# Kernel tuning notes

Measured on AMD Instinct MI355X. Metric: run time of the kernel, lower is better.

## Reference

```python
import jax, jax.numpy as jnp
import numpy as np

UNITS = 512
IN_DIM = 256
BATCH = 256
SEQ = 256


def setup_inputs() -> dict:
    key = jax.random.key(0)
    ks = jax.random.split(key, 9)
    s = lambda fan_in: 1.0 / np.sqrt(fan_in)
    inputs = jax.random.normal(ks[0], (BATCH, SEQ, IN_DIM), dtype=jnp.float32)
    # layer 0: input dim IN_DIM -> UNITS; layer 1: UNITS -> UNITS
    W0 = jax.random.normal(ks[1], (IN_DIM, 4 * UNITS), dtype=jnp.float32) * s(IN_DIM)
    U0 = jax.random.normal(ks[2], (UNITS, 4 * UNITS), dtype=jnp.float32) * s(UNITS)
    b0 = jnp.zeros((4 * UNITS,), dtype=jnp.float32)
    W1 = jax.random.normal(ks[3], (UNITS, 4 * UNITS), dtype=jnp.float32) * s(UNITS)
    U1 = jax.random.normal(ks[4], (UNITS, 4 * UNITS), dtype=jnp.float32) * s(UNITS)
    b1 = jnp.zeros((4 * UNITS,), dtype=jnp.float32)
    Wfc = jax.random.normal(ks[5], (UNITS, 1), dtype=jnp.float32) * s(UNITS)
    bfc = jnp.zeros((1,), dtype=jnp.float32)
    return {"inputs": inputs, "W0": W0, "U0": U0, "b0": b0,
            "W1": W1, "U1": U1, "b1": b1, "Wfc": Wfc, "bfc": bfc}


def _lstm_cell(x, h, c, W, U, b):
    # Keras LSTMCell gate order: i, f, g(candidate), o
    z = x @ W + h @ U + b  # [B, 4u]
    i, f, g, o = jnp.split(z, 4, axis=-1)
    c_new = jax.nn.sigmoid(f) * c + jax.nn.sigmoid(i) * jnp.tanh(g)
    h_new = jax.nn.sigmoid(o) * jnp.tanh(c_new)
    return h_new, c_new


def reference(inputs, W0, U0, b0, W1, U1, b1, Wfc, bfc):
    B = inputs.shape[0]
    u = U0.shape[0]
    zeros = jnp.zeros((B, u), dtype=inputs.dtype)
    init = (zeros, zeros, zeros, zeros)  # h0, c0, h1, c1

    def step(carry, x_t):
        h0, c0, h1, c1 = carry
        h0, c0 = _lstm_cell(x_t, h0, c0, W0, U0, b0)
        h1, c1 = _lstm_cell(h0, h1, c1, W1, U1, b1)
        return (h0, c0, h1, c1), None

    xs = jnp.swapaxes(inputs, 0, 1)  # [T, B, D]
    (h0, c0, h1, c1), _ = jax.lax.scan(step, init, xs)
    # RNN returns last output of top cell; Dense(1) head
    return h1 @ Wfc + bfc  # [B, 1]
```

## Files before the change

kernel.cpp:

```cpp
#include <hip/hip_runtime.h>
#include <hip/hip_bf16.h>

#define BATCH 256
#define SEQT  256
#define INDIM 256
#define UNITS 512
#define GCOLS 2048
#define BLOCKT 256

typedef __attribute__((ext_vector_type(8))) __bf16 bf16x8;
typedef __attribute__((ext_vector_type(4))) float  f32x4;

#define AS1 __attribute__((address_space(1)))
#define AS3 __attribute__((address_space(3)))

__device__ __forceinline__ void load_lds16_coh(const void* gsrc, void* ldst) {
    __builtin_amdgcn_global_load_lds((AS1 void*)gsrc, (AS3 void*)ldst, 16, 0, 0x11);
}

__device__ __forceinline__ float sigf(float x) { return 1.0f / (1.0f + __expf(-x)); }

__device__ __forceinline__ float tanhfast(float x) {
    float e = __expf(-2.0f * fabsf(x));
    float t = (1.0f - e) / (1.0f + e);
    return x < 0.0f ? -t : t;
}

__device__ __forceinline__ unsigned short f2bf(float f) {
    unsigned u = __float_as_uint(f);
    u += 0x7fffu + ((u >> 16) & 1u);
    return (unsigned short)(u >> 16);
}

__device__ __forceinline__ void st_coh(unsigned long long* p, unsigned long long v) {
    __hip_atomic_store(p, v, __ATOMIC_RELAXED, __HIP_MEMORY_SCOPE_AGENT);
}

__device__ __forceinline__ void group_barrier(unsigned* cnt, unsigned target) {
    asm volatile("s_waitcnt vmcnt(0)" ::: "memory");
    __syncthreads();
    if (threadIdx.x == 0) {
        __hip_atomic_fetch_add(cnt, 1u, __ATOMIC_RELAXED, __HIP_MEMORY_SCOPE_AGENT);
        while (__hip_atomic_load(cnt, __ATOMIC_RELAXED, __HIP_MEMORY_SCOPE_AGENT) < target)
            __builtin_amdgcn_s_sleep(1);
    }
    __syncthreads();
}

template <int LAYER>
__device__ void run_lstm(const float* __restrict__ X,
                         const float* __restrict__ Wx, const float* __restrict__ Ux,
                         const float* __restrict__ bias_v,
                         const float* __restrict__ Wfc, const float* __restrict__ bfc,
                         float* __restrict__ out, unsigned* __restrict__ cnt,
                         unsigned short* __restrict__ h0buf,
                         unsigned short* __restrict__ h1buf,
                         unsigned char* smem, int r0, int u0)
{
    constexpr int NKK = LAYER ? 32 : 24;
    constexpr int KS  = LAYER ? 16 : 8;

    const int tid  = threadIdx.x;
    const int lane = tid & 63;
    const int w    = tid >> 6;
    const int l16  = lane & 15;
    const int kb8  = (lane >> 4) * 8;
    const int col  = w * 512 + u0 + l16;
    float* gates   = (float*)(smem + 131072);

    bf16x8 bfrag[NKK];
#pragma unroll
    for (int kk = 0; kk < NKK; ++kk) {
        const float* srcm = (kk < KS)
            ? (Wx + (size_t)(kk * 32 + kb8) * GCOLS + col)
            : (Ux + (size_t)((kk - KS) * 32 + kb8) * GCOLS + col);
        bf16x8 v;
#pragma unroll
        for (int j = 0; j < 8; ++j) v[j] = (__bf16)srcm[(size_t)j * GCOLS];
        bfrag[kk] = v;
    }
    const float bias = bias_v[col];

    float c[4]  = {0.f, 0.f, 0.f, 0.f};
    float hn[4] = {0.f, 0.f, 0.f, 0.f};
    const int rl = lane;
    const int jb = w * 4;

    auto stage_x = [&](int t) {
#pragma unroll
        for (int i = 0; i < 8; ++i) {
            int f = w * 8 + i;
            int m = f & 3, kk = f >> 2;
            int row = r0 + m * 16 + l16;
            const float* sx = X + ((size_t)row * SEQT + t) * INDIM + kk * 32 + kb8;
            float4 x0 = *(const float4*)sx;
            float4 x1 = *(const float4*)(sx + 4);
            bf16x8 v;
            v[0] = (__bf16)x0.x; v[1] = (__bf16)x0.y; v[2] = (__bf16)x0.z; v[3] = (__bf16)x0.w;
            v[4] = (__bf16)x1.x; v[5] = (__bf16)x1.y; v[6] = (__bf16)x1.z; v[7] = (__bf16)x1.w;
            *(bf16x8*)(smem + (size_t)f * 1024 + lane * 16) = v;
        }
    };

    if (LAYER == 0) stage_x(0);
    __syncthreads();

#pragma unroll 1
    for (int s = 0; s <= SEQT; ++s) {
        const bool active = LAYER ? (s >= 1) : (s < SEQT);
        if (active) {
            const int rbuf = (s - 1) & 1, wbuf = s & 1;
            const unsigned short* h0r = h0buf + (size_t)rbuf * BATCH * UNITS;

            if (LAYER == 0) {
#pragma unroll
                for (int i = 0; i < 16; ++i) {
                    int f = 32 + w * 16 + i;
                    int m = f & 3, kk = f >> 2;
                    int row = r0 + m * 16 + l16;
                    load_lds16_coh(h0r + (size_t)row * UNITS + (kk - 8) * 32 + kb8,
                                   smem + (size_t)f * 1024);
                }
            } else {
                const unsigned short* h1r = h1buf + (size_t)rbuf * BATCH * UNITS;
#pragma unroll
                for (int i = 0; i < 32; ++i) {
                    int f = w * 32 + i;
                    int m = f & 3, kk = f >> 2;
                    int row = r0 + m * 16 + l16;
                    int k = kk * 32 + kb8;
                    const unsigned short* src = (k < 512)
                        ? (h0r + (size_t)row * UNITS + k)
                        : (h1r + (size_t)row * UNITS + (k - 512));
                    load_lds16_coh(src, smem + (size_t)f * 1024);
                }
            }

            f32x4 acc[4];
#pragma unroll
            for (int m = 0; m < 4; ++m) acc[m] = (f32x4){bias, bias, bias, bias};

            if (LAYER == 0) {
#pragma unroll
                for (int kk = 0; kk < 8; ++kk)
#pragma unroll
                    for (int m = 0; m < 4; ++m) {
                        bf16x8 a = *(const bf16x8*)(smem + (size_t)(kk * 4 + m) * 1024 + lane * 16);
                        acc[m] = __builtin_amdgcn_mfma_f32_16x16x32_bf16(a, bfrag[kk], acc[m], 0, 0, 0);
                    }
            }

            asm volatile("s_waitcnt vmcnt(0)" ::: "memory");
            __syncthreads();

            {
                constexpr int K0 = LAYER ? 0 : 8;
#pragma unroll
                for (int kk = K0; kk < NKK; ++kk)
#pragma unroll
                    for (int m = 0; m < 4; ++m) {
                        bf16x8 a = *(const bf16x8*)(smem + (size_t)(kk * 4 + m) * 1024 + lane * 16);
                        acc[m] = __builtin_amdgcn_mfma_f32_16x16x32_bf16(a, bfrag[kk], acc[m], 0, 0, 0);
                    }
            }

#pragma unroll
            for (int m = 0; m < 4; ++m)
#pragma unroll
                for (int r = 0; r < 4; ++r)
                    gates[(w * 64 + m * 16 + (lane >> 4) * 4 + r) * 17 + l16] = acc[m][r];
            __syncthreads();

            unsigned short hb4[4];
#pragma unroll
            for (int j = 0; j < 4; ++j) {
                int ul = jb + j;
                float zi = gates[(0 * 64 + rl) * 17 + ul];
                float zf = gates[(1 * 64 + rl) * 17 + ul];
                float zg = gates[(2 * 64 + rl) * 17 + ul];
                float zo = gates[(3 * 64 + rl) * 17 + ul];
                float cn = sigf(zf) * c[j] + sigf(zi) * tanhfast(zg);
                float h  = sigf(zo) * tanhfast(cn);
                c[j] = cn; hn[j] = h; hb4[j] = f2bf(h);
            }
            if (!(LAYER == 1 && s == SEQT)) {
                unsigned short* hw = (LAYER ? h1buf : h0buf)
                    + (size_t)wbuf * BATCH * UNITS + (size_t)(r0 + rl) * UNITS + u0 + jb;
                unsigned long long hv = (unsigned long long)hb4[0]
                                      | ((unsigned long long)hb4[1] << 16)
                                      | ((unsigned long long)hb4[2] << 32)
                                      | ((unsigned long long)hb4[3] << 48);
                st_coh((unsigned long long*)hw, hv);
            }

            if (LAYER == 0 && s + 1 < SEQT) stage_x(s + 1);
        }
        if (s < SEQT) group_barrier(cnt, 64u * (unsigned)(s + 1));
    }

    if (LAYER == 1) {
        float p = hn[0] * Wfc[u0 + jb + 0] + hn[1] * Wfc[u0 + jb + 1]
                + hn[2] * Wfc[u0 + jb + 2] + hn[3] * Wfc[u0 + jb + 3];
        if (u0 == 0 && jb == 0) p += bfc[0];
        atomicAdd(out + r0 + rl, p);
    }
}

__global__ void __launch_bounds__(BLOCKT, 1)
lstm_kernel(const float* __restrict__ X,
            const float* __restrict__ W0, const float* __restrict__ U0, const float* __restrict__ b0,
            const float* __restrict__ W1, const float* __restrict__ U1, const float* __restrict__ b1,
            const float* __restrict__ Wfc, const float* __restrict__ bfc,
            float* __restrict__ out, unsigned* __restrict__ counters,
            unsigned short* __restrict__ h0buf, unsigned short* __restrict__ h1buf)
{
    __shared__ __align__(16) unsigned char smem[148480];
    const int G = (int)blockIdx.x & 7;
    const int S = (int)blockIdx.x >> 3;
    const int r0 = (G & 3) * 64;
    const int u0 = S * 16;
    unsigned* cnt = counters + (G & 3) * 64;
    if (G < 4)
        run_lstm<0>(X, W0, U0, b0, Wfc, bfc, out, cnt, h0buf, h1buf, smem, r0, u0);
    else
        run_lstm<1>(X, W1, U1, b1, Wfc, bfc, out, cnt, h0buf, h1buf, smem, r0, u0);
}

extern "C" void kernel_launch(void* const* d_in, const int* in_sizes, int n_in,
                              void* d_out, int out_size, void* d_ws, size_t ws_size,
                              hipStream_t stream) {
    (void)in_sizes; (void)n_in; (void)out_size; (void)ws_size;
    const float* X   = (const float*)d_in[0];
    const float* W0  = (const float*)d_in[1];
    const float* U0  = (const float*)d_in[2];
    const float* b0  = (const float*)d_in[3];
    const float* W1  = (const float*)d_in[4];
    const float* U1  = (const float*)d_in[5];
    const float* b1  = (const float*)d_in[6];
    const float* Wfc = (const float*)d_in[7];
    const float* bfc = (const float*)d_in[8];
    float* out = (float*)d_out;

    unsigned char* ws = (unsigned char*)d_ws;
    unsigned* counters     = (unsigned*)ws;
    unsigned short* h0buf  = (unsigned short*)(ws + 1024);
    unsigned short* h1buf  = (unsigned short*)(ws + 1024 + 2 * BATCH * UNITS * 2);

    hipMemsetAsync(d_ws, 0, 1024 + 4 * BATCH * UNITS * 2, stream);
    hipMemsetAsync(d_out, 0, BATCH * sizeof(float), stream);

    lstm_kernel<<<dim3(256), dim3(BLOCKT), 0, stream>>>(
        X, W0, U0, b0, W1, U1, b1, Wfc, bfc, out, counters, h0buf, h1buf);
}
```

Baseline: 2.761 ms.

## Replace group counter barrier with per-block progress slots and 4-deep h buffers

Replaces the shared atomic-counter barrier across the 64 blocks of each batch group with per-block progress slots. Each block publishes its step number, and before a step a wavefront polls all 64 slots in parallel. Layer 0 now waits only on its own layer's previous step and on layer 1 two steps back, so the two layers can drift apart, which the move to 4-deep h0/h1 ring buffers allows. The aim is to cut lockstep stalls and atomic contention, in exchange for more polling traffic and more workspace memory.

```diff
diff --git a/kernel.cpp b/kernel.cpp
--- a/kernel.cpp
+++ b/kernel.cpp
@@ -35,16 +35,16 @@
 __device__ __forceinline__ void st_coh(unsigned long long* p, unsigned long long v) {
     __hip_atomic_store(p, v, __ATOMIC_RELAXED, __HIP_MEMORY_SCOPE_AGENT);
 }
-
-__device__ __forceinline__ void group_barrier(unsigned* cnt, unsigned target) {
-    asm volatile("s_waitcnt vmcnt(0)" ::: "memory");
-    __syncthreads();
-    if (threadIdx.x == 0) {
-        __hip_atomic_fetch_add(cnt, 1u, __ATOMIC_RELAXED, __HIP_MEMORY_SCOPE_AGENT);
-        while (__hip_atomic_load(cnt, __ATOMIC_RELAXED, __HIP_MEMORY_SCOPE_AGENT) < target)
-            __builtin_amdgcn_s_sleep(1);
-    }
-    __syncthreads();
+__device__ __forceinline__ void slot_store(unsigned* p, unsigned v) {
+    __hip_atomic_store(p, v, __ATOMIC_RELAXED, __HIP_MEMORY_SCOPE_AGENT);
+}
+
+__device__ __forceinline__ void slot_wait(const unsigned* slots, int tgt0, int tgt1) {
+    if (tgt0 <= 0 && tgt1 <= 0) return;
+    const int l = (int)(threadIdx.x & 63);
+    const unsigned* p = slots + l * 4;
+    const int tgt = (l < 32) ? tgt0 : tgt1;
+    while (!__all((int)__hip_atomic_load(p, __ATOMIC_RELAXED, __HIP_MEMORY_SCOPE_AGENT) >= tgt)) {}
 }
 
 template <int LAYER>
@@ -52,7 +52,7 @@
                          const float* __restrict__ Wx, const float* __restrict__ Ux,
                          const float* __restrict__ bias_v,
                          const float* __restrict__ Wfc, const float* __restrict__ bfc,
-                         float* __restrict__ out, unsigned* __restrict__ cnt,
+                         float* __restrict__ out, unsigned* __restrict__ slots, int myslot,
                          unsigned short* __restrict__ h0buf,
                          unsigned short* __restrict__ h1buf,
                          unsigned char* smem, int r0, int u0)
@@ -105,12 +105,15 @@
     if (LAYER == 0) stage_x(0);
     __syncthreads();
 
+    const int SMAX = LAYER ? SEQT : (SEQT - 1);
 #pragma unroll 1
-    for (int s = 0; s <= SEQT; ++s) {
-        const bool active = LAYER ? (s >= 1) : (s < SEQT);
+    for (int s = 0; s <= SMAX; ++s) {
+        const bool active = LAYER ? (s >= 1) : true;
         if (active) {
-            const int rbuf = (s - 1) & 1, wbuf = s & 1;
+            const int rbuf = (s + 3) & 3, wbuf = s & 3;
             const unsigned short* h0r = h0buf + (size_t)rbuf * BATCH * UNITS;
+
+            slot_wait(slots, s, LAYER ? s : s - 2);
 
             if (LAYER == 0) {
 #pragma unroll
@@ -192,10 +195,13 @@
                                       | ((unsigned long long)hb4[3] << 48);
                 st_coh((unsigned long long*)hw, hv);
             }
-
-            if (LAYER == 0 && s + 1 < SEQT) stage_x(s + 1);
+            asm volatile("s_waitcnt vmcnt(0)" ::: "memory");
+            __syncthreads();
         }
-        if (s < SEQT) group_barrier(cnt, 64u * (unsigned)(s + 1));
+
+        if (tid == 0) slot_store(slots + myslot * 4, (unsigned)(s + 1));
+        if (LAYER == 0 && s + 1 <= SMAX) stage_x(s + 1);
+        __syncthreads();
     }
 
     if (LAYER == 1) {
@@ -211,7 +217,7 @@
             const float* __restrict__ W0, const float* __restrict__ U0, const float* __restrict__ b0,
             const float* __restrict__ W1, const float* __restrict__ U1, const float* __restrict__ b1,
             const float* __restrict__ Wfc, const float* __restrict__ bfc,
-            float* __restrict__ out, unsigned* __restrict__ counters,
+            float* __restrict__ out, unsigned* __restrict__ slots,
             unsigned short* __restrict__ h0buf, unsigned short* __restrict__ h1buf)
 {
     __shared__ __align__(16) unsigned char smem[148480];
@@ -219,11 +225,12 @@
     const int S = (int)blockIdx.x >> 3;
     const int r0 = (G & 3) * 64;
     const int u0 = S * 16;
-    unsigned* cnt = counters + (G & 3) * 64;
+    unsigned* gslots = slots + (G & 3) * 256;
+    const int myslot = (G < 4 ? 0 : 32) + S;
     if (G < 4)
-        run_lstm<0>(X, W0, U0, b0, Wfc, bfc, out, cnt, h0buf, h1buf, smem, r0, u0);
+        run_lstm<0>(X, W0, U0, b0, Wfc, bfc, out, gslots, myslot, h0buf, h1buf, smem, r0, u0);
     else
-        run_lstm<1>(X, W1, U1, b1, Wfc, bfc, out, cnt, h0buf, h1buf, smem, r0, u0);
+        run_lstm<1>(X, W1, U1, b1, Wfc, bfc, out, gslots, myslot, h0buf, h1buf, smem, r0, u0);
 }
 
 extern "C" void kernel_launch(void* const* d_in, const int* in_sizes, int n_in,
@@ -242,13 +249,13 @@
     float* out = (float*)d_out;
 
     unsigned char* ws = (unsigned char*)d_ws;
-    unsigned* counters     = (unsigned*)ws;
-    unsigned short* h0buf  = (unsigned short*)(ws + 1024);
-    unsigned short* h1buf  = (unsigned short*)(ws + 1024 + 2 * BATCH * UNITS * 2);
-
-    hipMemsetAsync(d_ws, 0, 1024 + 4 * BATCH * UNITS * 2, stream);
+    unsigned* slots        = (unsigned*)ws;
+    unsigned short* h0buf  = (unsigned short*)(ws + 4096);
+    unsigned short* h1buf  = (unsigned short*)(ws + 4096 + 4 * BATCH * UNITS * 2);
+
+    hipMemsetAsync(d_ws, 0, 4096 + 8 * BATCH * UNITS * 2, stream);
     hipMemsetAsync(d_out, 0, BATCH * sizeof(float), stream);
 
     lstm_kernel<<<dim3(256), dim3(BLOCKT), 0, stream>>>(
-        X, W0, U0, b0, W1, U1, b1, Wfc, bfc, out, counters, h0buf, h1buf);
-}
+        X, W0, U0, b0, W1, U1, b1, Wfc, bfc, out, slots, h0buf, h1buf);
+}
```

New measurement: 2.800 ms. Within noise of the previous version (+1.4%).
